# Performance work log

Hardware: AMD Instinct MI355X
Metric: run time of the kernel (lower is better)

The kernel has to match this reference:

```python
import math
import jax, jax.numpy as jnp
import numpy as np

DIM = 1024
H = 16
DH = DIM // H
B = 4
T = 1024


def setup_inputs() -> dict:
    key = jax.random.key(0)
    ks = jax.random.split(key, 16)
    s = 0.02
    return {
        "x": jax.random.normal(ks[0], (B, T, DIM), jnp.float32),
        "pos": jax.random.normal(ks[1], (1, T, DIM), jnp.float32),
        "mask": jnp.ones((B, T, T), dtype=bool),
        "Wq": jax.random.normal(ks[2], (DIM, DIM), jnp.float32) * s,
        "bq": jax.random.normal(ks[3], (DIM,), jnp.float32) * s,
        "Wk": jax.random.normal(ks[4], (DIM, DIM), jnp.float32) * s,
        "bk": jax.random.normal(ks[5], (DIM,), jnp.float32) * s,
        "Wv": jax.random.normal(ks[6], (DIM, DIM), jnp.float32) * s,
        "bv": jax.random.normal(ks[7], (DIM,), jnp.float32) * s,
        "Wp": jax.random.normal(ks[8], (DIM, DIM), jnp.float32) * s,
        "Wo": jax.random.normal(ks[9], (DIM, DIM), jnp.float32) * s,
        "bo": jax.random.normal(ks[10], (DIM,), jnp.float32) * s,
        "pos_bias_u": jax.random.normal(ks[11], (H, DH), jnp.float32) * s,
        "pos_bias_v": jax.random.normal(ks[12], (H, DH), jnp.float32) * s,
    }


def _shape(y):
    # [b, t, dim] -> [b, h, t, dh]
    b, t, _ = y.shape
    return y.reshape(b, t, H, DH).transpose(0, 2, 1, 3)


def _relative_shift(x):
    # x: [b, h, tq, tk]
    b, h, tq, tk = x.shape
    x = jnp.pad(x, ((0, 0), (0, 0), (0, 0), (1, 0)))  # zero col at front
    x = x.reshape(b, h, tk + 1, tq)[:, :, 1:, :]
    return x.reshape(b, h, tq, tk)


def reference(x, pos, mask, Wq, bq, Wk, bk, Wv, bv, Wp, Wo, bo, pos_bias_u, pos_bias_v):
    q = _shape(jnp.einsum("btd,ed->bte", x, Wq) + bq)      # [b,h,t,dh]
    k = _shape(jnp.einsum("btd,ed->bte", x, Wk) + bk)
    v = _shape(jnp.einsum("btd,ed->bte", x, Wv) + bv)
    p = _shape(jnp.einsum("btd,ed->bte", pos, Wp))          # [1,h,t,dh]

    q_u = q + pos_bias_u[None, :, None, :]
    q_v = q + pos_bias_v[None, :, None, :]

    content = jnp.einsum("bhqd,bhkd->bhqk", q_u, k)
    position = jnp.einsum("bhqd,xhkd->bhqk", q_v, p)        # broadcast pos batch
    position = _relative_shift(position)[..., : content.shape[-1]]

    scores = (content + position) / math.sqrt(DH)
    scores = jnp.where(mask[:, None, :, :], scores, -1e9)
    attn = jax.nn.softmax(scores, axis=-1)

    ctx = jnp.einsum("bhqk,bhkd->bhqd", attn, v)
    ctx = ctx.transpose(0, 2, 1, 3).reshape(x.shape[0], x.shape[1], DIM)
    return jnp.einsum("btd,ed->bte", ctx, Wo) + bo
```

## Files before the change

kernel.cpp:

```cpp
#include <hip/hip_runtime.h>
#include <hip/hip_bf16.h>

#define DIMc 1024
#define Hc   16
#define DHc  64
#define Bc   4
#define Tc   1024

typedef __attribute__((ext_vector_type(8))) short s16x8;
typedef __attribute__((ext_vector_type(4))) short s16x4;
typedef __attribute__((ext_vector_type(4))) float f32x4;

__device__ inline short f2bf(float x) {
  unsigned u = __float_as_uint(x);
  u += 0x7fffu + ((u >> 16) & 1u);
  return (short)(u >> 16);
}
__device__ inline float bf2f(short s) {
  return __uint_as_float(((unsigned)(unsigned short)s) << 16);
}
__device__ inline unsigned cvtpk(float lo, float hi) {
  unsigned r;
  asm("v_cvt_pk_bf16_f32 %0, %1, %2" : "=v"(r) : "v"(lo), "v"(hi));
  return r;
}

#define MFMA16(a, b, c) __builtin_amdgcn_mfma_f32_16x16x32_bf16((a), (b), (c), 0, 0, 0)

__device__ __forceinline__ void gl16(const short* g, short* l) {
  __builtin_amdgcn_global_load_lds(
      (const __attribute__((address_space(1))) unsigned int*)g,
      (__attribute__((address_space(3))) unsigned int*)l, 16, 0, 0);
}

__global__ __launch_bounds__(256) void cast_f32_bf16(const float* __restrict__ in,
                                                     short* __restrict__ out, int n) {
  const int i = (blockIdx.x * 256 + threadIdx.x) * 8;
  if (i >= n) return;
  const float4 a = *(const float4*)(in + i);
  const float4 b = *(const float4*)(in + i + 4);
  s16x8 r;
  r[0] = f2bf(a.x); r[1] = f2bf(a.y); r[2] = f2bf(a.z); r[3] = f2bf(a.w);
  r[4] = f2bf(b.x); r[5] = f2bf(b.y); r[6] = f2bf(b.z); r[7] = f2bf(b.w);
  *(s16x8*)(out + i) = r;
}

__global__ __launch_bounds__(256) void cast6_f32_bf16(
    const float* s0, const float* s1, const float* s2, const float* s3,
    const float* s4, const float* s5,
    short* d0, short* d1, short* d2, short* d3, short* d4, short* d5) {
  const float* sp[6] = {s0, s1, s2, s3, s4, s5};
  short* dp[6] = {d0, d1, d2, d3, d4, d5};
  const int z = blockIdx.z;
  const float* in = sp[z];
  short* out = dp[z];
  const int i = (blockIdx.x * 256 + threadIdx.x) * 8;
  const float4 a = *(const float4*)(in + i);
  const float4 b = *(const float4*)(in + i + 4);
  s16x8 r;
  r[0] = f2bf(a.x); r[1] = f2bf(a.y); r[2] = f2bf(a.z); r[3] = f2bf(a.w);
  r[4] = f2bf(b.x); r[5] = f2bf(b.y); r[6] = f2bf(b.z); r[7] = f2bf(b.w);
  *(s16x8*)(out + i) = r;
}

__device__ __forceinline__ void gemm_core(const short* __restrict__ Ab,
                                          const short* __restrict__ Bb,
                                          int bm, int bn,
                                          short (*As)[4096], short (*Bs)[4096],
                                          f32x4 (&acc)[4][4]) {
  const int tid = threadIdx.x;
  const int w = tid >> 6, l = tid & 63;
  const int wr = w >> 1, wc = w & 1;
  const int ll = l & 15, lg = l >> 4;

  const int r0 = (w * 128 + l) >> 2;
  const int ksw = ((l & 3) ^ ((l >> 2) & 3)) * 8;
  const short* pA0 = Ab + (size_t)(bm + r0) * 1024 + ksw;
  const short* pA1 = Ab + (size_t)(bm + r0 + 16) * 1024 + ksw;
  const short* pB0 = Bb + (size_t)(bn + r0) * 1024 + ksw;
  const short* pB1 = Bb + (size_t)(bn + r0 + 16) * 1024 + ksw;
  const int lb = w * 1024;

  gl16(pA0, &As[0][lb]);
  gl16(pA1, &As[0][lb + 512]);
  gl16(pB0, &Bs[0][lb]);
  gl16(pB1, &Bs[0][lb + 512]);
  __syncthreads();

  const int kcA = ((lg ^ (ll & 3)) * 8);
  int cur = 0;
  for (int k0 = 0; k0 < 1024; k0 += 32) {
    if (k0 + 32 < 1024) {
      const int nx = cur ^ 1;
      gl16(pA0 + k0 + 32, &As[nx][lb]);
      gl16(pA1 + k0 + 32, &As[nx][lb + 512]);
      gl16(pB0 + k0 + 32, &Bs[nx][lb]);
      gl16(pB1 + k0 + 32, &Bs[nx][lb + 512]);
    }
    s16x8 af[4], bf_[4];
#pragma unroll
    for (int i = 0; i < 4; ++i) {
      af[i]  = *(const s16x8*)&As[cur][(wr * 64 + i * 16 + ll) * 32 + kcA];
      bf_[i] = *(const s16x8*)&Bs[cur][(wc * 64 + i * 16 + ll) * 32 + kcA];
    }
    __builtin_amdgcn_s_setprio(1);
#pragma unroll
    for (int mi = 0; mi < 4; ++mi)
#pragma unroll
      for (int ni = 0; ni < 4; ++ni)
        acc[mi][ni] = MFMA16(af[mi], bf_[ni], acc[mi][ni]);
    __builtin_amdgcn_s_setprio(0);
    __syncthreads();
    cur ^= 1;
  }
}

__global__ __launch_bounds__(256) void proj_all(
    const short* __restrict__ xb, const short* __restrict__ pb,
    const short* __restrict__ Wqb, const short* __restrict__ Wkb,
    const short* __restrict__ Wvb, const short* __restrict__ Wpb,
    const float* __restrict__ bq, const float* __restrict__ bk,
    const float* __restrict__ bv,
    const float* __restrict__ pbu, const float* __restrict__ pbv,
    short* __restrict__ Quw, short* __restrict__ Qvw,
    short* __restrict__ Kw, short* __restrict__ Vw,
    short* __restrict__ P2o) {
  const int z = blockIdx.z;
  if (z == 3 && blockIdx.x >= 8) return;
  __shared__ __align__(16) short LDSu[17408];
  short (*As)[4096] = (short (*)[4096])(LDSu);
  short (*Bs)[4096] = (short (*)[4096])(LDSu + 8192);

  const short* Ab = (z == 3) ? pb : xb;
  const short* Bb = (z == 0) ? Wqb : (z == 1) ? Wkb : (z == 2) ? Wvb : Wpb;

  f32x4 acc[4][4];
#pragma unroll
  for (int i = 0; i < 4; ++i)
#pragma unroll
    for (int j = 0; j < 4; ++j) acc[i][j] = (f32x4){0.f, 0.f, 0.f, 0.f};

  const int bm = blockIdx.x * 128, bn = blockIdx.y * 128;
  gemm_core(Ab, Bb, bm, bn, As, Bs, acc);

  const int tid = threadIdx.x;
  const int w = tid >> 6, l = tid & 63;
  const int wr = w >> 1, wc = w & 1;
  const int ll = l & 15, lg = l >> 4;

  if (z == 2) {
    short* T = LDSu;
#pragma unroll
    for (int mi = 0; mi < 4; ++mi)
#pragma unroll
      for (int ni = 0; ni < 4; ++ni) {
        const int col = wc * 64 + ni * 16 + ll;
        const int row0 = wr * 64 + mi * 16 + lg * 4;
        const float bias = bv[bn + col];
        s16x4 t4;
#pragma unroll
        for (int r = 0; r < 4; ++r) t4[r] = f2bf(acc[mi][ni][r] + bias);
        *(s16x4*)&T[col * 136 + row0] = t4;
      }
    __syncthreads();
    const int b_ = bm >> 10;
    const int t0 = bm & 1023;
#pragma unroll
    for (int i = 0; i < 4; ++i) {
      const int c2 = tid + i * 256;
      const int colL = c2 >> 3;
      const int rb = (c2 & 7) * 16;
      const s16x8 v0 = *(const s16x8*)&T[colL * 136 + rb];
      const s16x8 v1 = *(const s16x8*)&T[colL * 136 + rb + 8];
      const int gcol = bn + colL;
      const int hh = gcol >> 6, dh = gcol & 63;
      short* dst = Vw + (((size_t)b_ * Hc + hh) * DHc + dh) * Tc + t0 + rb;
      *(s16x8*)dst = v0;
      *(s16x8*)(dst + 8) = v1;
    }
    return;
  }

#pragma unroll
  for (int mi = 0; mi < 4; ++mi)
#pragma unroll
    for (int ni = 0; ni < 4; ++ni)
#pragma unroll
      for (int r = 0; r < 4; ++r) {
        const int row = bm + wr * 64 + mi * 16 + lg * 4 + r;
        const int col = bn + wc * 64 + ni * 16 + ll;
        float v = acc[mi][ni][r];
        if (z == 3) {
          const int hh = col >> 6, dh = col & 63;
          const short v16 = f2bf(v);
          short* P2h = P2o + ((size_t)hh * 2048) * DHc;
          P2h[(size_t)row * DHc + dh] = v16;
          if (row <= 1021) P2h[(size_t)(1025 + row) * DHc + dh] = v16;
          if (row == 1023) P2h[(size_t)1024 * DHc + dh] = 0;
          if (row == 1022) P2h[(size_t)2047 * DHc + dh] = 0;
        } else {
          const int b_ = row >> 10, t = row & 1023, hh = col >> 6, dh = col & 63;
          const size_t o = (((size_t)b_ * Hc + hh) * Tc + t) * DHc + dh;
          if (z == 0) {
            v += bq[col];
            Quw[o] = f2bf((v + pbu[col]) * 0.125f);
            Qvw[o] = f2bf((v + pbv[col]) * 0.125f);
          } else {
            Kw[o] = f2bf(v + bk[col]);
          }
        }
      }
}

__global__ __launch_bounds__(256) void wo_gemm(const short* __restrict__ A,
                                               const short* __restrict__ B,
                                               const float* __restrict__ bias,
                                               float* __restrict__ Cf) {
  __shared__ __align__(16) short As[2][4096];
  __shared__ __align__(16) short Bs[2][4096];
  f32x4 acc[4][4];
#pragma unroll
  for (int i = 0; i < 4; ++i)
#pragma unroll
    for (int j = 0; j < 4; ++j) acc[i][j] = (f32x4){0.f, 0.f, 0.f, 0.f};

  const int bm = blockIdx.x * 128, bn = blockIdx.y * 128;
  gemm_core(A, B, bm, bn, As, Bs, acc);

  const int tid = threadIdx.x;
  const int w = tid >> 6, l = tid & 63;
  const int wr = w >> 1, wc = w & 1;
  const int ll = l & 15, lg = l >> 4;
#pragma unroll
  for (int mi = 0; mi < 4; ++mi)
#pragma unroll
    for (int ni = 0; ni < 4; ++ni)
#pragma unroll
      for (int r = 0; r < 4; ++r) {
        const int row = bm + wr * 64 + mi * 16 + lg * 4 + r;
        const int col = bn + wc * 64 + ni * 16 + ll;
        Cf[(size_t)row * DIMc + col] = acc[mi][ni][r] + bias[col];
      }
}

__global__ __launch_bounds__(256) void flash_attn(
    const short* __restrict__ Qu, const short* __restrict__ Qv,
    const short* __restrict__ Kg, const short* __restrict__ VTg,
    const short* __restrict__ P2, short* __restrict__ ctx) {
  __shared__ __align__(16) short L[14976];
  short* Kt  = L;
  short* Vt  = L + 4608;
  short* U   = L + 9216;

  const int tid = threadIdx.x;
  const int w = tid >> 6, l = tid & 63;
  const int ll = l & 15, lg = l >> 4;
  const int orig = blockIdx.x + (blockIdx.y << 4) + (blockIdx.z << 8);
  const int wg = (orig & 7) * 128 + (orig >> 3);
  const int qt = wg & 15, h = (wg >> 4) & 15, b = wg >> 8;
  const int q0 = qt * 64;

  const size_t bh = (size_t)b * Hc + h;
  const short* Qup = Qu + (bh * Tc + q0) * DHc;
  const short* Qvp = Qv + (bh * Tc + q0) * DHc;
  const short* Kgp = Kg + bh * Tc * DHc;
  const short* VTp = VTg + bh * DHc * Tc;
  const short* P2h = P2 + (size_t)h * 2048 * DHc;

  s16x8 qau[2], qav[2], qav1[2];
  {
    const short* qr  = Qup + (size_t)(w * 16 + ll) * 64;
    const short* qvr = Qvp + (size_t)(w * 16 + ll) * 64;
#pragma unroll
    for (int ks = 0; ks < 2; ++ks) {
      qau[ks]  = *(const s16x8*)(qr + ks * 32 + lg * 8);
      qav[ks]  = *(const s16x8*)(qvr + ks * 32 + lg * 8);
      qav1[ks] = *(const s16x8*)(qvr + 64 + ks * 32 + lg * 8);
    }
  }

  f32x4 o[4];
#pragma unroll
  for (int cd = 0; cd < 4; ++cd) o[cd] = (f32x4){0.f, 0.f, 0.f, 0.f};
  float m_run[4], l_run[4];
#pragma unroll
  for (int r = 0; r < 4; ++r) { m_run[r] = -3.0e38f; l_run[r] = 0.f; }

  const int ci2lo = 3 - w;
  const int spwb = w * 1440;

  s16x8 kr[2], vr[2], pf[2][5];
  auto issue_kv = [&](int kt) {
#pragma unroll
    for (int i = 0; i < 2; ++i) {
      const int c = tid + i * 256;
      const int row = c >> 3, col8 = (c & 7) * 8;
      kr[i] = *(const s16x8*)(Kgp + (size_t)(kt * 64 + row) * 64 + col8);
      vr[i] = *(const s16x8*)(VTp + (size_t)row * Tc + kt * 64 + col8);
    }
  };
  auto issue_pos = [&](int kt) {
    const int wb = (kt - qt) * 64 + 960;
#pragma unroll
    for (int j = 0; j < 5; ++j) {
      const short* pr = P2h + (size_t)(wb + (ci2lo + j) * 16 + ll) * 64 + lg * 8;
      pf[0][j] = *(const s16x8*)(pr);
      pf[1][j] = *(const s16x8*)(pr + 32);
    }
  };
  issue_kv(0);
  issue_pos(0);

  for (int kt = 0; kt < 16; ++kt) {
    const int dtile = kt - qt;
    __syncthreads();
#pragma unroll
    for (int i = 0; i < 2; ++i) {
      const int c = tid + i * 256;
      const int row = c >> 3, col8 = (c & 7) * 8;
      *(s16x8*)&Kt[row * 72 + col8] = kr[i];
      *(s16x8*)&Vt[row * 72 + (col8 ^ (((row >> 3) & 3) << 3))] = vr[i];
    }
    __syncthreads();
    if (kt < 15) issue_kv(kt + 1);

    f32x4 s[4];
#pragma unroll
    for (int ci = 0; ci < 4; ++ci) s[ci] = (f32x4){0.f, 0.f, 0.f, 0.f};
#pragma unroll
    for (int ks = 0; ks < 2; ++ks) {
      s16x8 kb[4];
#pragma unroll
      for (int ci = 0; ci < 4; ++ci)
        kb[ci] = *(const s16x8*)&Kt[(ci * 16 + ll) * 72 + ks * 32 + lg * 8];
      __builtin_amdgcn_s_setprio(1);
#pragma unroll
      for (int ci = 0; ci < 4; ++ci) s[ci] = MFMA16(qau[ks], kb[ci], s[ci]);
      __builtin_amdgcn_s_setprio(0);
    }

    if (dtile <= 0) {
      f32x4 pc[5];
#pragma unroll
      for (int j = 0; j < 5; ++j) pc[j] = (f32x4){0.f, 0.f, 0.f, 0.f};
#pragma unroll
      for (int ks = 0; ks < 2; ++ks) {
        __builtin_amdgcn_s_setprio(1);
#pragma unroll
        for (int j = 0; j < 5; ++j) pc[j] = MFMA16(qav[ks], pf[ks][j], pc[j]);
        __builtin_amdgcn_s_setprio(0);
      }
#pragma unroll
      for (int j = 0; j < 5; ++j) {
        const int ba = spwb + (j * 16 + ll) * 18 + lg * 4;
        *(unsigned*)&U[ba]     = cvtpk(pc[j][0], pc[j][1]);
        *(unsigned*)&U[ba + 2] = cvtpk(pc[j][2], pc[j][3]);
      }
      asm volatile("s_waitcnt lgkmcnt(0)" ::: "memory");
#pragma unroll
      for (int ci = 0; ci < 4; ++ci)
#pragma unroll
        for (int r = 0; r < 4; ++r) {
          const int rel = ci * 16 + ll - w * 16 - lg * 4 - r;
          if (dtile < 0 || rel <= 0)
            s[ci][r] += bf2f(U[spwb + (rel + w * 16 + 15) * 18 + lg * 4 + r]);
        }
      asm volatile("s_waitcnt lgkmcnt(0)" ::: "memory");
    }
    if (dtile >= 0) {
      f32x4 pc[5];
#pragma unroll
      for (int j = 0; j < 5; ++j) pc[j] = (f32x4){0.f, 0.f, 0.f, 0.f};
#pragma unroll
      for (int ks = 0; ks < 2; ++ks) {
        __builtin_amdgcn_s_setprio(1);
#pragma unroll
        for (int j = 0; j < 5; ++j) pc[j] = MFMA16(qav1[ks], pf[ks][j], pc[j]);
        __builtin_amdgcn_s_setprio(0);
      }
#pragma unroll
      for (int j = 0; j < 5; ++j) {
        const int ba = spwb + (j * 16 + ll) * 18 + lg * 4;
        *(unsigned*)&U[ba]     = cvtpk(pc[j][0], pc[j][1]);
        *(unsigned*)&U[ba + 2] = cvtpk(pc[j][2], pc[j][3]);
      }
      asm volatile("s_waitcnt lgkmcnt(0)" ::: "memory");
#pragma unroll
      for (int ci = 0; ci < 4; ++ci)
#pragma unroll
        for (int r = 0; r < 4; ++r) {
          const int rel = ci * 16 + ll - w * 16 - lg * 4 - r;
          if (dtile > 0 || rel >= 1)
            s[ci][r] += bf2f(U[spwb + (rel + w * 16 + 15) * 18 + lg * 4 + r]);
        }
      asm volatile("s_waitcnt lgkmcnt(0)" ::: "memory");
    }
    if (kt < 15) issue_pos(kt + 1);

    float fac[4];
#pragma unroll
    for (int r = 0; r < 4; ++r) {
      float mx = fmaxf(fmaxf(s[0][r], s[1][r]), fmaxf(s[2][r], s[3][r]));
      mx = fmaxf(mx, __shfl_xor(mx, 1));
      mx = fmaxf(mx, __shfl_xor(mx, 2));
      mx = fmaxf(mx, __shfl_xor(mx, 4));
      mx = fmaxf(mx, __shfl_xor(mx, 8));
      const float mnew = fmaxf(m_run[r], mx);
      const float f = __expf(m_run[r] - mnew);
      float lsum = 0.f;
#pragma unroll
      for (int ci = 0; ci < 4; ++ci) {
        const float e = __expf(s[ci][r] - mnew);
        s[ci][r] = e;
        lsum += e;
      }
      lsum += __shfl_xor(lsum, 1);
      lsum += __shfl_xor(lsum, 2);
      lsum += __shfl_xor(lsum, 4);
      lsum += __shfl_xor(lsum, 8);
      m_run[r] = mnew;
      l_run[r] = l_run[r] * f + lsum;
      fac[r] = f;
    }
#pragma unroll
    for (int cd = 0; cd < 4; ++cd)
#pragma unroll
      for (int r = 0; r < 4; ++r) o[cd][r] *= fac[r];

#pragma unroll
    for (int ci = 0; ci < 4; ++ci) {
      const unsigned p01 = cvtpk(s[ci][0], s[ci][1]);
      const unsigned p23 = cvtpk(s[ci][2], s[ci][3]);
      const int base = spwb + lg * 4 * 72 + ci * 16 + ll;
      U[base]           = (short)p01;
      U[base + 72]      = (short)(p01 >> 16);
      U[base + 144]     = (short)p23;
      U[base + 216]     = (short)(p23 >> 16);
    }
    asm volatile("s_waitcnt lgkmcnt(0)" ::: "memory");

#pragma unroll
    for (int ks = 0; ks < 2; ++ks) {
      s16x8 pa = *(const s16x8*)&U[spwb + ll * 72 + ks * 32 + lg * 8];
      s16x8 vv[4];
#pragma unroll
      for (int cd = 0; cd < 4; ++cd) {
        const int d = cd * 16 + ll;
        const int key8 = ks * 32 + lg * 8;
        vv[cd] = *(const s16x8*)&Vt[d * 72 + (key8 ^ (((d >> 3) & 3) << 3))];
      }
      __builtin_amdgcn_s_setprio(1);
#pragma unroll
      for (int cd = 0; cd < 4; ++cd) o[cd] = MFMA16(pa, vv[cd], o[cd]);
      __builtin_amdgcn_s_setprio(0);
    }
  }

#pragma unroll
  for (int r = 0; r < 4; ++r) {
    const float inv = 1.f / l_run[r];
    const int row = q0 + w * 16 + lg * 4 + r;
#pragma unroll
    for (int cd = 0; cd < 4; ++cd) {
      const int d = cd * 16 + ll;
      ctx[((size_t)b * Tc + row) * DIMc + h * DHc + d] = f2bf(o[cd][r] * inv);
    }
  }
}

extern "C" void kernel_launch(void* const* d_in, const int* in_sizes, int n_in,
                              void* d_out, int out_size, void* d_ws,
                              size_t ws_size, hipStream_t stream) {
  const float* x   = (const float*)d_in[0];
  const float* pos = (const float*)d_in[1];
  const float* Wq  = (const float*)d_in[3];
  const float* bq  = (const float*)d_in[4];
  const float* Wk  = (const float*)d_in[5];
  const float* bk  = (const float*)d_in[6];
  const float* Wv  = (const float*)d_in[7];
  const float* bv  = (const float*)d_in[8];
  const float* Wp  = (const float*)d_in[9];
  const float* Wo  = (const float*)d_in[10];
  const float* bo  = (const float*)d_in[11];
  const float* pbu = (const float*)d_in[12];
  const float* pbv = (const float*)d_in[13];
  float* out = (float*)d_out;

  char* ws = (char*)d_ws;
  const size_t MB = 1024 * 1024;
  short* xb  = (short*)(ws + 0 * MB);
  short* pb  = (short*)(ws + 8 * MB);
  short* Wqb = (short*)(ws + 10 * MB);
  short* Wkb = (short*)(ws + 12 * MB);
  short* Wvb = (short*)(ws + 14 * MB);
  short* Wpb = (short*)(ws + 16 * MB);
  short* Wob = (short*)(ws + 18 * MB);
  short* Quw = (short*)(ws + 20 * MB);
  short* Qvw = (short*)(ws + 28 * MB);
  short* Kw  = (short*)(ws + 36 * MB);
  short* Vw  = (short*)(ws + 44 * MB);
  short* P2w_ = (short*)(ws + 52 * MB);
  short* Cw  = (short*)(ws + 56 * MB);

  const dim3 blk(256);
  hipLaunchKernelGGL(cast_f32_bf16, dim3(2048), blk, 0, stream, x, xb, 4194304);
  hipLaunchKernelGGL(cast6_f32_bf16, dim3(512, 1, 6), blk, 0, stream,
                     pos, Wq, Wk, Wv, Wp, Wo, pb, Wqb, Wkb, Wvb, Wpb, Wob);

  hipLaunchKernelGGL(proj_all, dim3(32, 8, 4), blk, 0, stream,
                     xb, pb, Wqb, Wkb, Wvb, Wpb, bq, bk, bv, pbu, pbv,
                     Quw, Qvw, Kw, Vw, P2w_);
  hipLaunchKernelGGL(flash_attn, dim3(16, 16, 4), blk, 0, stream,
                     Quw, Qvw, Kw, Vw, P2w_, Cw);
  hipLaunchKernelGGL(wo_gemm, dim3(32, 8), blk, 0, stream, Cw, Wob, bo, out);
}
```

Measured before the change: 193.7 us.

## Process two 64-key tiles per flash-attention iteration with doubled LDS staging

The flash attention loop now handles 128 keys per iteration. It stages two K/V tiles in shared memory, computes eight score fragments, and does one online-softmax rescale per pair instead of per tile. The positional fragment prefetch is moved inside the pos pass, so it issues right after the MFMAs consume the registers. This halves barriers and softmax max/rescale overhead, at the cost of more LDS (about 48KB), more registers for prefetched K/V, and possibly lower occupancy.

```diff
diff --git a/kernel.cpp b/kernel.cpp
--- a/kernel.cpp
+++ b/kernel.cpp
@@ -247,10 +247,8 @@
     const short* __restrict__ Qu, const short* __restrict__ Qv,
     const short* __restrict__ Kg, const short* __restrict__ VTg,
     const short* __restrict__ P2, short* __restrict__ ctx) {
-  __shared__ __align__(16) short L[14976];
-  short* Kt  = L;
-  short* Vt  = L + 4608;
-  short* U   = L + 9216;
+  __shared__ __align__(16) short L[24192];
+  short* U = L + 18432;
 
   const int tid = threadIdx.x;
   const int w = tid >> 6, l = tid & 63;
@@ -289,18 +287,22 @@
   const int ci2lo = 3 - w;
   const int spwb = w * 1440;
 
-  s16x8 kr[2], vr[2], pf[2][5];
-  auto issue_kv = [&](int kt) {
-#pragma unroll
-    for (int i = 0; i < 2; ++i) {
-      const int c = tid + i * 256;
-      const int row = c >> 3, col8 = (c & 7) * 8;
-      kr[i] = *(const s16x8*)(Kgp + (size_t)(kt * 64 + row) * 64 + col8);
-      vr[i] = *(const s16x8*)(VTp + (size_t)row * Tc + kt * 64 + col8);
+  s16x8 kr[4], vr[4], pf[2][5];
+  auto issue_kv = [&](int kt2) {
+#pragma unroll
+    for (int st = 0; st < 2; ++st) {
+      const int key0 = (kt2 * 2 + st) * 64;
+#pragma unroll
+      for (int i = 0; i < 2; ++i) {
+        const int c = tid + i * 256;
+        const int row = c >> 3, col8 = (c & 7) * 8;
+        kr[st * 2 + i] = *(const s16x8*)(Kgp + (size_t)(key0 + row) * 64 + col8);
+        vr[st * 2 + i] = *(const s16x8*)(VTp + (size_t)row * Tc + key0 + col8);
+      }
     }
   };
-  auto issue_pos = [&](int kt) {
-    const int wb = (kt - qt) * 64 + 960;
+  auto issue_pos = [&](int st_abs) {
+    const int wb = (st_abs - qt) * 64 + 960;
 #pragma unroll
     for (int j = 0; j < 5; ++j) {
       const short* pr = P2h + (size_t)(wb + (ci2lo + j) * 16 + ll) * 64 + lg * 8;
@@ -311,35 +313,46 @@
   issue_kv(0);
   issue_pos(0);
 
-  for (int kt = 0; kt < 16; ++kt) {
-    const int dtile = kt - qt;
+  for (int kt2 = 0; kt2 < 8; ++kt2) {
+    const int st0 = kt2 * 2, st1 = st0 + 1;
     __syncthreads();
 #pragma unroll
-    for (int i = 0; i < 2; ++i) {
-      const int c = tid + i * 256;
-      const int row = c >> 3, col8 = (c & 7) * 8;
-      *(s16x8*)&Kt[row * 72 + col8] = kr[i];
-      *(s16x8*)&Vt[row * 72 + (col8 ^ (((row >> 3) & 3) << 3))] = vr[i];
+    for (int st = 0; st < 2; ++st) {
+      short* KtS = L + st * 9216;
+      short* VtS = L + 4608 + st * 9216;
+#pragma unroll
+      for (int i = 0; i < 2; ++i) {
+        const int c = tid + i * 256;
+        const int row = c >> 3, col8 = (c & 7) * 8;
+        *(s16x8*)&KtS[row * 72 + col8] = kr[st * 2 + i];
+        *(s16x8*)&VtS[row * 72 + (col8 ^ (((row >> 3) & 3) << 3))] = vr[st * 2 + i];
+      }
     }
     __syncthreads();
-    if (kt < 15) issue_kv(kt + 1);
-
-    f32x4 s[4];
-#pragma unroll
-    for (int ci = 0; ci < 4; ++ci) s[ci] = (f32x4){0.f, 0.f, 0.f, 0.f};
-#pragma unroll
-    for (int ks = 0; ks < 2; ++ks) {
-      s16x8 kb[4];
-#pragma unroll
-      for (int ci = 0; ci < 4; ++ci)
-        kb[ci] = *(const s16x8*)&Kt[(ci * 16 + ll) * 72 + ks * 32 + lg * 8];
-      __builtin_amdgcn_s_setprio(1);
-#pragma unroll
-      for (int ci = 0; ci < 4; ++ci) s[ci] = MFMA16(qau[ks], kb[ci], s[ci]);
-      __builtin_amdgcn_s_setprio(0);
-    }
-
-    if (dtile <= 0) {
+    if (kt2 < 7) issue_kv(kt2 + 1);
+
+    f32x4 s[8];
+#pragma unroll
+    for (int ci = 0; ci < 8; ++ci) s[ci] = (f32x4){0.f, 0.f, 0.f, 0.f};
+#pragma unroll
+    for (int st = 0; st < 2; ++st) {
+      const short* KtS = L + st * 9216;
+#pragma unroll
+      for (int ks = 0; ks < 2; ++ks) {
+        s16x8 kb[4];
+#pragma unroll
+        for (int ci = 0; ci < 4; ++ci)
+          kb[ci] = *(const s16x8*)&KtS[(ci * 16 + ll) * 72 + ks * 32 + lg * 8];
+        __builtin_amdgcn_s_setprio(1);
+#pragma unroll
+        for (int ci = 0; ci < 4; ++ci)
+          s[st * 4 + ci] = MFMA16(qau[ks], kb[ci], s[st * 4 + ci]);
+        __builtin_amdgcn_s_setprio(0);
+      }
+    }
+
+    auto pos_pass = [&](const s16x8 (&qa)[2], int dtile, int mode, int soff,
+                        int issue_st) {
       f32x4 pc[5];
 #pragma unroll
       for (int j = 0; j < 5; ++j) pc[j] = (f32x4){0.f, 0.f, 0.f, 0.f};
@@ -347,9 +360,10 @@
       for (int ks = 0; ks < 2; ++ks) {
         __builtin_amdgcn_s_setprio(1);
 #pragma unroll
-        for (int j = 0; j < 5; ++j) pc[j] = MFMA16(qav[ks], pf[ks][j], pc[j]);
+        for (int j = 0; j < 5; ++j) pc[j] = MFMA16(qa[ks], pf[ks][j], pc[j]);
         __builtin_amdgcn_s_setprio(0);
       }
+      if (issue_st >= 0) issue_pos(issue_st);
 #pragma unroll
       for (int j = 0; j < 5; ++j) {
         const int ba = spwb + (j * 16 + ll) * 18 + lg * 4;
@@ -362,45 +376,26 @@
 #pragma unroll
         for (int r = 0; r < 4; ++r) {
           const int rel = ci * 16 + ll - w * 16 - lg * 4 - r;
-          if (dtile < 0 || rel <= 0)
-            s[ci][r] += bf2f(U[spwb + (rel + w * 16 + 15) * 18 + lg * 4 + r]);
+          const bool use = (mode == 0) ? (dtile < 0 || rel <= 0)
+                                       : (dtile > 0 || rel >= 1);
+          if (use)
+            s[soff + ci][r] += bf2f(U[spwb + (rel + w * 16 + 15) * 18 + lg * 4 + r]);
         }
       asm volatile("s_waitcnt lgkmcnt(0)" ::: "memory");
-    }
-    if (dtile >= 0) {
-      f32x4 pc[5];
-#pragma unroll
-      for (int j = 0; j < 5; ++j) pc[j] = (f32x4){0.f, 0.f, 0.f, 0.f};
-#pragma unroll
-      for (int ks = 0; ks < 2; ++ks) {
-        __builtin_amdgcn_s_setprio(1);
-#pragma unroll
-        for (int j = 0; j < 5; ++j) pc[j] = MFMA16(qav1[ks], pf[ks][j], pc[j]);
-        __builtin_amdgcn_s_setprio(0);
-      }
-#pragma unroll
-      for (int j = 0; j < 5; ++j) {
-        const int ba = spwb + (j * 16 + ll) * 18 + lg * 4;
-        *(unsigned*)&U[ba]     = cvtpk(pc[j][0], pc[j][1]);
-        *(unsigned*)&U[ba + 2] = cvtpk(pc[j][2], pc[j][3]);
-      }
-      asm volatile("s_waitcnt lgkmcnt(0)" ::: "memory");
-#pragma unroll
-      for (int ci = 0; ci < 4; ++ci)
-#pragma unroll
-        for (int r = 0; r < 4; ++r) {
-          const int rel = ci * 16 + ll - w * 16 - lg * 4 - r;
-          if (dtile > 0 || rel >= 1)
-            s[ci][r] += bf2f(U[spwb + (rel + w * 16 + 15) * 18 + lg * 4 + r]);
-        }
-      asm volatile("s_waitcnt lgkmcnt(0)" ::: "memory");
-    }
-    if (kt < 15) issue_pos(kt + 1);
+    };
+    const int nst = (kt2 < 7) ? st0 + 2 : -1;
+    const int d0 = st0 - qt, d1 = st1 - qt;
+    if (d0 <= 0) pos_pass(qav,  d0, 0, 0, (d0 >= 0) ? -1 : st1);
+    if (d0 >= 0) pos_pass(qav1, d0, 1, 0, st1);
+    if (d1 <= 0) pos_pass(qav,  d1, 0, 4, (d1 >= 0) ? -1 : nst);
+    if (d1 >= 0) pos_pass(qav1, d1, 1, 4, nst);
 
     float fac[4];
 #pragma unroll
     for (int r = 0; r < 4; ++r) {
-      float mx = fmaxf(fmaxf(s[0][r], s[1][r]), fmaxf(s[2][r], s[3][r]));
+      float mx = s[0][r];
+#pragma unroll
+      for (int ci = 1; ci < 8; ++ci) mx = fmaxf(mx, s[ci][r]);
       mx = fmaxf(mx, __shfl_xor(mx, 1));
       mx = fmaxf(mx, __shfl_xor(mx, 2));
       mx = fmaxf(mx, __shfl_xor(mx, 4));
@@ -409,7 +404,7 @@
       const float f = __expf(m_run[r] - mnew);
       float lsum = 0.f;
 #pragma unroll
-      for (int ci = 0; ci < 4; ++ci) {
+      for (int ci = 0; ci < 8; ++ci) {
         const float e = __expf(s[ci][r] - mnew);
         s[ci][r] = e;
         lsum += e;
@@ -428,31 +423,35 @@
       for (int r = 0; r < 4; ++r) o[cd][r] *= fac[r];
 
 #pragma unroll
-    for (int ci = 0; ci < 4; ++ci) {
-      const unsigned p01 = cvtpk(s[ci][0], s[ci][1]);
-      const unsigned p23 = cvtpk(s[ci][2], s[ci][3]);
-      const int base = spwb + lg * 4 * 72 + ci * 16 + ll;
-      U[base]           = (short)p01;
-      U[base + 72]      = (short)(p01 >> 16);
-      U[base + 144]     = (short)p23;
-      U[base + 216]     = (short)(p23 >> 16);
-    }
-    asm volatile("s_waitcnt lgkmcnt(0)" ::: "memory");
-
-#pragma unroll
-    for (int ks = 0; ks < 2; ++ks) {
-      s16x8 pa = *(const s16x8*)&U[spwb + ll * 72 + ks * 32 + lg * 8];
-      s16x8 vv[4];
-#pragma unroll
-      for (int cd = 0; cd < 4; ++cd) {
-        const int d = cd * 16 + ll;
-        const int key8 = ks * 32 + lg * 8;
-        vv[cd] = *(const s16x8*)&Vt[d * 72 + (key8 ^ (((d >> 3) & 3) << 3))];
-      }
-      __builtin_amdgcn_s_setprio(1);
-#pragma unroll
-      for (int cd = 0; cd < 4; ++cd) o[cd] = MFMA16(pa, vv[cd], o[cd]);
-      __builtin_amdgcn_s_setprio(0);
+    for (int st = 0; st < 2; ++st) {
+      const short* VtS = L + 4608 + st * 9216;
+#pragma unroll
+      for (int ci = 0; ci < 4; ++ci) {
+        const unsigned p01 = cvtpk(s[st * 4 + ci][0], s[st * 4 + ci][1]);
+        const unsigned p23 = cvtpk(s[st * 4 + ci][2], s[st * 4 + ci][3]);
+        const int base = spwb + lg * 4 * 72 + ci * 16 + ll;
+        U[base]       = (short)p01;
+        U[base + 72]  = (short)(p01 >> 16);
+        U[base + 144] = (short)p23;
+        U[base + 216] = (short)(p23 >> 16);
+      }
+      asm volatile("s_waitcnt lgkmcnt(0)" ::: "memory");
+#pragma unroll
+      for (int ks = 0; ks < 2; ++ks) {
+        s16x8 pa = *(const s16x8*)&U[spwb + ll * 72 + ks * 32 + lg * 8];
+        s16x8 vv[4];
+#pragma unroll
+        for (int cd = 0; cd < 4; ++cd) {
+          const int d = cd * 16 + ll;
+          const int key8 = ks * 32 + lg * 8;
+          vv[cd] = *(const s16x8*)&VtS[d * 72 + (key8 ^ (((d >> 3) & 3) << 3))];
+        }
+        __builtin_amdgcn_s_setprio(1);
+#pragma unroll
+        for (int cd = 0; cd < 4; ++cd) o[cd] = MFMA16(pa, vv[cd], o[cd]);
+        __builtin_amdgcn_s_setprio(0);
+      }
+      asm volatile("s_waitcnt lgkmcnt(0)" ::: "memory");
     }
   }
 
```

New measurement: 257.9 us. 33.1% more time.
